# Kernel optimization log

Hardware: AMD Instinct MI355X
Metric: run time of the kernel (lower is better)

The kernel has to match this reference:

```python
import jax, jax.numpy as jnp
import numpy as np

D = 1024   # hidden_dim
F = 4096   # ffn_dim
E = 8      # expert_num
K = 2      # top_k
B, S = 2, 2048

def setup_inputs() -> dict:
    key = jax.random.key(0)
    ks = jax.random.split(key, 5)
    scale = 0.02
    x = jax.random.normal(ks[0], (B, S, D), dtype=jnp.float32)
    gate_w = jax.random.normal(ks[1], (D, E), dtype=jnp.float32) * scale
    w1 = jax.random.normal(ks[2], (E, D, F), dtype=jnp.float32) * scale
    w3 = jax.random.normal(ks[3], (E, D, F), dtype=jnp.float32) * scale
    w2 = jax.random.normal(ks[4], (E, F, D), dtype=jnp.float32) * scale
    return {"x": x, "gate_w": gate_w, "w1": w1, "w3": w3, "w2": w2}

def reference(x, gate_w, w1, w3, w2):
    # x: [B, S, D] -> tokens [T, D]
    Bb, Ss, Dd = x.shape
    xt = x.reshape(-1, Dd)                                  # [T, D]
    T = xt.shape[0]
    # Router: softmax over experts in float32 (matches torch dtype=torch.float)
    router_probs = jax.nn.softmax((xt @ gate_w).astype(jnp.float32), axis=-1)  # [T, E]
    topk_w, topk_idx = jax.lax.top_k(router_probs, K)        # [T, K]
    topk_w = topk_w / topk_w.sum(axis=-1, keepdims=True)
    topk_w = topk_w.astype(x.dtype)
    # Combine weights scattered to dense [T, E] (equivalent to per-expert gather/scatter loop)
    combine = jnp.zeros((T, E), dtype=x.dtype).at[jnp.arange(T)[:, None], topk_idx].add(topk_w)
    # SwishFFN per expert: w2(silu(x w1) * (x w3)), no bias
    h = jax.nn.silu(jnp.einsum('td,edf->etf', xt, w1)) * jnp.einsum('td,edf->etf', xt, w3)  # [E, T, F]
    out_e = jnp.einsum('etf,efd->etd', h, w2)                # [E, T, D]
    out = jnp.einsum('etd,te->td', out_e, combine)           # [T, D]
    return out.reshape(Bb, Ss, Dd), router_probs
```

## Files before the change

### kernel.cpp

```cpp
#include <hip/hip_runtime.h>

typedef unsigned short u16;
typedef unsigned int u32;
typedef __attribute__((ext_vector_type(8))) short bf16x8;
typedef __attribute__((ext_vector_type(4))) float f32x4;
typedef __attribute__((ext_vector_type(4))) int i32x4;
typedef __attribute__((ext_vector_type(2))) unsigned int u32x2;


__device__ __forceinline__ u16 f2bf(float f) {
  u32 u = __builtin_bit_cast(u32, f);
  u += 0x7fffu + ((u >> 16) & 1u);
  return (u16)(u >> 16);
}
__device__ __forceinline__ u32 pack2(u16 a, u16 b) { return (u32)a | ((u32)b << 16); }

__device__ __forceinline__ char* lds_swz(void* base, int row, int byteInRow) {
  return (char*)base + (((row << 7) + byteInRow) ^ ((row & 7) << 4));
}

#define GLL16(g, l) __builtin_amdgcn_global_load_lds( \
    (const __attribute__((address_space(1))) void*)(g), \
    (__attribute__((address_space(3))) void*)(l), 16, 0, 0)

__global__ __launch_bounds__(256) void router_k(
    const float* __restrict__ x, const float* __restrict__ gw,
    float* __restrict__ probs, u16* __restrict__ xb,
    float* __restrict__ wa, int* __restrict__ alist, int* __restrict__ cnt)
{
  const int t = blockIdx.x;
  const int tid = threadIdx.x;
  f32x4 xv = ((const f32x4*)(x + (size_t)t * 1024))[tid];
  u32x2 hb;
  hb[0] = pack2(f2bf(xv[0]), f2bf(xv[1]));
  hb[1] = pack2(f2bf(xv[2]), f2bf(xv[3]));
  *(u32x2*)(xb + (size_t)t * 1024 + tid * 4) = hb;

  float acc[8];
#pragma unroll
  for (int e = 0; e < 8; ++e) acc[e] = 0.f;
  const float* g = gw + tid * 32;
#pragma unroll
  for (int j = 0; j < 4; ++j)
#pragma unroll
    for (int e = 0; e < 8; ++e) acc[e] = fmaf(xv[j], g[j * 8 + e], acc[e]);

#pragma unroll
  for (int e = 0; e < 8; ++e)
    for (int off = 32; off > 0; off >>= 1) acc[e] += __shfl_down(acc[e], off);

  __shared__ float red[4][8];
  const int lane = tid & 63, wid = tid >> 6;
  if (lane == 0) {
#pragma unroll
    for (int e = 0; e < 8; ++e) red[wid][e] = acc[e];
  }
  __syncthreads();
  if (tid == 0) {
    float p[8]; float mx = -1e30f;
#pragma unroll
    for (int e = 0; e < 8; ++e) { p[e] = red[0][e] + red[1][e] + red[2][e] + red[3][e]; mx = fmaxf(mx, p[e]); }
    float s = 0.f;
#pragma unroll
    for (int e = 0; e < 8; ++e) { p[e] = __expf(p[e] - mx); s += p[e]; }
    float inv = 1.f / s;
#pragma unroll
    for (int e = 0; e < 8; ++e) { p[e] *= inv; probs[(size_t)t * 8 + e] = p[e]; }
    int i0 = 0;
#pragma unroll
    for (int e = 1; e < 8; ++e) if (p[e] > p[i0]) i0 = e;
    int i1 = (i0 == 0) ? 1 : 0;
#pragma unroll
    for (int e = 0; e < 8; ++e) if (e != i0 && p[e] > p[i1]) i1 = e;
    float s2 = p[i0] + p[i1];
    int pos0 = atomicAdd(&cnt[i0], 1); alist[i0 * 4096 + pos0] = t * 2;
    int pos1 = atomicAdd(&cnt[i1], 1); alist[i1 * 4096 + pos1] = t * 2 + 1;
    wa[t * 2]     = p[i0] / s2;
    wa[t * 2 + 1] = p[i1] / s2;
  }
}

__global__ __launch_bounds__(256) void wtrans_k(const float* __restrict__ src, u16* __restrict__ dst,
                                               int R, int C)
{
  const int e = blockIdx.z;
  src += (size_t)e * R * C;
  dst += (size_t)e * R * C;
  const int c0 = blockIdx.x * 64, r0 = blockIdx.y * 64;
  __shared__ u16 t[64][72];
  const int tid = threadIdx.x;
  const int rr = (tid >> 4) * 4, cc = (tid & 15) * 4;
  f32x4 v[4];
#pragma unroll
  for (int j = 0; j < 4; ++j) v[j] = *(const f32x4*)(src + (size_t)(r0 + rr + j) * C + c0 + cc);
#pragma unroll
  for (int c = 0; c < 4; ++c) {
    u32x2 p;
    p[0] = pack2(f2bf(v[0][c]), f2bf(v[1][c]));
    p[1] = pack2(f2bf(v[2][c]), f2bf(v[3][c]));
    *(u32x2*)&t[cc + c][rr] = p;
  }
  __syncthreads();
  const int c = tid >> 2, rs = (tid & 3) * 16;
  i32x4 a0 = *(const i32x4*)&t[c][rs];
  i32x4 a1 = *(const i32x4*)&t[c][rs + 8];
  u16* dp = dst + (size_t)(c0 + c) * R + r0 + rs;
  *(i32x4*)dp = a0;
  *(i32x4*)(dp + 8) = a1;
}

__global__ __launch_bounds__(256, 2) void gemm1_k(
    const u16* __restrict__ xb, const u16* __restrict__ w1t, const u16* __restrict__ w3t,
    const int* __restrict__ alist, const int* __restrict__ cnt, u16* __restrict__ H)
{
  const int e = blockIdx.z;
  const int mc = cnt[e];
  const int m0 = blockIdx.y * 128;
  if (m0 >= mc) return;
  const int n0 = blockIdx.x * 64;
  const int tid = threadIdx.x;

  __shared__ u16 As[128 * 64];
  __shared__ u16 Bs[2][64 * 64];
  __shared__ int rowid[128];

  if (tid < 128) rowid[tid] = (m0 + tid < mc) ? alist[e * 4096 + m0 + tid] : -1;
  __syncthreads();

  const int l = tid & 63, w = tid >> 6;
  const u16* wt = (w >> 1) ? w3t : w1t;
  u16* bbase = &Bs[w >> 1][0];

  const u16* aps[4]; const u16* bps[4];
  u16* ald[4]; u16* bld[4];
#pragma unroll
  for (int q = 0; q < 4; ++q) {
    int ra = 32 * w + 8 * q + (l >> 3);
    int id = rowid[ra];
    aps[q] = xb + (size_t)(id < 0 ? 0 : (id >> 1)) * 1024 + ((l & 7) ^ (ra & 7)) * 8;
    ald[q] = As + (32 * w + 8 * q) * 64;
    int rb = 32 * (w & 1) + 8 * q + (l >> 3);
    bps[q] = wt + (size_t)e * 4194304 + (size_t)(n0 + rb) * 1024 + ((l & 7) ^ (rb & 7)) * 8;
    bld[q] = bbase + (32 * (w & 1) + 8 * q) * 64;
  }

  const int wm = (w >> 1) * 64, wn = (w & 1) * 32;
  const int l15 = l & 15, lg = l >> 4;

  f32x4 acc1[4][2], acc3[4][2];
  const f32x4 zf = {0.f, 0.f, 0.f, 0.f};
#pragma unroll
  for (int mi = 0; mi < 4; ++mi) { acc1[mi][0] = zf; acc1[mi][1] = zf; acc3[mi][0] = zf; acc3[mi][1] = zf; }

  for (int kt = 0; kt < 16; ++kt) {
    const int ko = kt * 64;
#pragma unroll
    for (int q = 0; q < 4; ++q) GLL16(aps[q] + ko, ald[q]);
#pragma unroll
    for (int q = 0; q < 4; ++q) GLL16(bps[q] + ko, bld[q]);
    __syncthreads();
#pragma unroll
    for (int ks = 0; ks < 2; ++ks) {
      const int kb = ks * 64 + lg * 16;
      bf16x8 af[4];
#pragma unroll
      for (int mi = 0; mi < 4; ++mi)
        af[mi] = *(const bf16x8*)lds_swz(As, wm + mi * 16 + l15, kb);
#pragma unroll
      for (int ni = 0; ni < 2; ++ni) {
        bf16x8 b1 = *(const bf16x8*)lds_swz(&Bs[0][0], wn + ni * 16 + l15, kb);
        bf16x8 b3 = *(const bf16x8*)lds_swz(&Bs[1][0], wn + ni * 16 + l15, kb);
#pragma unroll
        for (int mi = 0; mi < 4; ++mi) {
          acc1[mi][ni] = __builtin_amdgcn_mfma_f32_16x16x32_bf16(af[mi], b1, acc1[mi][ni], 0, 0, 0);
          acc3[mi][ni] = __builtin_amdgcn_mfma_f32_16x16x32_bf16(af[mi], b3, acc3[mi][ni], 0, 0, 0);
        }
      }
    }
    __syncthreads();
  }

#pragma unroll
  for (int mi = 0; mi < 4; ++mi) {
    const int rb = wm + mi * 16 + lg * 4;
#pragma unroll
    for (int ni = 0; ni < 2; ++ni) {
      const int col = n0 + wn + ni * 16 + l15;
      f32x4 c1 = acc1[mi][ni], c3 = acc3[mi][ni];
#pragma unroll
      for (int j = 0; j < 4; ++j) {
        int id = rowid[rb + j];
        if (id >= 0) {
          float a = c1[j];
          float h = (a / (1.f + __expf(-a))) * c3[j];
          H[(size_t)id * 4096 + col] = f2bf(h);
        }
      }
    }
  }
}

__global__ __launch_bounds__(256, 2) void gemm2_k(
    const u16* __restrict__ H, const u16* __restrict__ w2t,
    const int* __restrict__ alist, const int* __restrict__ cnt,
    const float* __restrict__ wa, float* __restrict__ out)
{
  const int e = blockIdx.z;
  const int mc = cnt[e];
  const int yy = blockIdx.y;
  const int kh = yy & 1;
  const int m0 = (yy >> 1) * 128;
  if (m0 >= mc) return;
  const int n0 = blockIdx.x * 128;
  const int tid = threadIdx.x;

  __shared__ u16 As[128 * 64];
  __shared__ u16 Bs[128 * 64];
  __shared__ int rowid[128];
  __shared__ float rw[128];

  if (tid < 128) {
    int id = (m0 + tid < mc) ? alist[e * 4096 + m0 + tid] : -1;
    rowid[tid] = id;
    rw[tid] = (id >= 0) ? wa[id] : 0.f;
  }
  __syncthreads();

  const int l = tid & 63, w = tid >> 6;
  const size_t kbase = (size_t)kh * 2048;
  const u16* aps[4]; const u16* bps[4];
  u16* ald[4]; u16* bld[4];
#pragma unroll
  for (int q = 0; q < 4; ++q) {
    int ra = 32 * w + 8 * q + (l >> 3);
    int id = rowid[ra];
    aps[q] = H + (size_t)(id < 0 ? 0 : id) * 4096 + kbase + ((l & 7) ^ (ra & 7)) * 8;
    ald[q] = As + (32 * w + 8 * q) * 64;
    int rb = 32 * w + 8 * q + (l >> 3);
    bps[q] = w2t + (size_t)e * 4194304 + (size_t)(n0 + rb) * 4096 + kbase + ((l & 7) ^ (rb & 7)) * 8;
    bld[q] = Bs + (32 * w + 8 * q) * 64;
  }

  const int wm = (w >> 1) * 64, wn = (w & 1) * 64;
  const int l15 = l & 15, lg = l >> 4;

  f32x4 acc[4][4];
  const f32x4 zf = {0.f, 0.f, 0.f, 0.f};
#pragma unroll
  for (int mi = 0; mi < 4; ++mi)
#pragma unroll
    for (int ni = 0; ni < 4; ++ni) acc[mi][ni] = zf;

  for (int kt = 0; kt < 32; ++kt) {
    const int ko = kt * 64;
#pragma unroll
    for (int q = 0; q < 4; ++q) GLL16(aps[q] + ko, ald[q]);
#pragma unroll
    for (int q = 0; q < 4; ++q) GLL16(bps[q] + ko, bld[q]);
    __syncthreads();
#pragma unroll
    for (int ks = 0; ks < 2; ++ks) {
      const int kb = ks * 64 + lg * 16;
      bf16x8 af[4];
#pragma unroll
      for (int mi = 0; mi < 4; ++mi)
        af[mi] = *(const bf16x8*)lds_swz(As, wm + mi * 16 + l15, kb);
#pragma unroll
      for (int ni = 0; ni < 4; ++ni) {
        bf16x8 bfb = *(const bf16x8*)lds_swz(Bs, wn + ni * 16 + l15, kb);
#pragma unroll
        for (int mi = 0; mi < 4; ++mi)
          acc[mi][ni] = __builtin_amdgcn_mfma_f32_16x16x32_bf16(af[mi], bfb, acc[mi][ni], 0, 0, 0);
      }
    }
    __syncthreads();
  }

#pragma unroll
  for (int mi = 0; mi < 4; ++mi) {
    const int rb = wm + mi * 16 + lg * 4;
#pragma unroll
    for (int ni = 0; ni < 4; ++ni) {
      const int col = n0 + wn + ni * 16 + l15;
      f32x4 c = acc[mi][ni];
#pragma unroll
      for (int j = 0; j < 4; ++j) {
        int rr = rb + j;
        int id = rowid[rr];
        if (id >= 0)
          unsafeAtomicAdd(&out[(size_t)(id >> 1) * 1024 + col], c[j] * rw[rr]);
      }
    }
  }
}

extern "C" void kernel_launch(void* const* d_in, const int* in_sizes, int n_in,
                              void* d_out, int out_size, void* d_ws, size_t ws_size,
                              hipStream_t stream)
{
  (void)in_sizes; (void)n_in; (void)out_size; (void)ws_size;
  const float* x  = (const float*)d_in[0];
  const float* gw = (const float*)d_in[1];
  const float* w1 = (const float*)d_in[2];
  const float* w3 = (const float*)d_in[3];
  const float* w2 = (const float*)d_in[4];
  float* out   = (float*)d_out;
  float* probs = out + (size_t)4096 * 1024;

  const size_t MB = (size_t)1 << 20;
  char* ws = (char*)d_ws;
  u16*   xb    = (u16*)(ws);
  u16*   H     = (u16*)(ws + 8 * MB);
  u16*   w1t   = (u16*)(ws + 72 * MB);
  u16*   w3t   = (u16*)(ws + 136 * MB);
  u16*   w2t   = (u16*)(ws + 200 * MB);
  float* wa    = (float*)(ws + 264 * MB);
  int*   alist = (int*)(ws + 264 * MB + 32768);
  int*   cnt   = (int*)(ws + 264 * MB + 32768 + 131072);

  hipMemsetAsync(cnt, 0, 8 * sizeof(int), stream);
  hipMemsetAsync(out, 0, (size_t)4096 * 1024 * sizeof(float), stream);
  wtrans_k<<<dim3(64, 16, 8), 256, 0, stream>>>(w1, w1t, 1024, 4096);
  wtrans_k<<<dim3(64, 16, 8), 256, 0, stream>>>(w3, w3t, 1024, 4096);
  wtrans_k<<<dim3(16, 64, 8), 256, 0, stream>>>(w2, w2t, 4096, 1024);
  router_k<<<4096, 256, 0, stream>>>(x, gw, probs, xb, wa, alist, cnt);
  gemm1_k<<<dim3(64, 32, 8), 256, 0, stream>>>(xb, w1t, w3t, alist, cnt, H);
  gemm2_k<<<dim3(8, 64, 8), 256, 0, stream>>>(H, w2t, alist, cnt, wa, out);
}
```

Baseline: 501.3 us.

## Double-buffer weight tiles and register-prefetch gathered A rows in both expert GEMMs

Both expert GEMM kernels move from a single-buffered load-sync-compute loop to a software pipeline. B tiles are double-buffered in LDS through async global-to-LDS loads. A rows are prefetched into registers and written to LDS after compute, so memory latency overlaps the MFMA work. The three weight-transpose launches are merged into one kernel and the occupancy hint goes from 2 to 3 blocks. The cost is more LDS per block, hand-written waitcnt counts that must match the compiler's load ordering, and register pressure that may cause spills at the higher occupancy target.

```diff
diff --git a/kernel.cpp b/kernel.cpp
--- a/kernel.cpp
+++ b/kernel.cpp
@@ -80,13 +80,31 @@
   }
 }
 
-__global__ __launch_bounds__(256) void wtrans_k(const float* __restrict__ src, u16* __restrict__ dst,
-                                               int R, int C)
-{
-  const int e = blockIdx.z;
-  src += (size_t)e * R * C;
-  dst += (size_t)e * R * C;
-  const int c0 = blockIdx.x * 64, r0 = blockIdx.y * 64;
+__global__ __launch_bounds__(256) void wprep_k(
+    const float* __restrict__ w1, const float* __restrict__ w3, const float* __restrict__ w2,
+    u16* __restrict__ w1t, u16* __restrict__ w3t, u16* __restrict__ w2t)
+{
+  const int bid = blockIdx.x;
+  const float* src; u16* dst; int R, C, x, y, e;
+  if (bid < 16384) {
+    int sel = bid >> 13;
+    int t0 = bid & 8191;
+    e = t0 >> 10;
+    int rem = t0 & 1023;
+    x = rem & 63; y = rem >> 6;
+    R = 1024; C = 4096;
+    src = (sel ? w3 : w1); dst = (sel ? w3t : w1t);
+  } else {
+    int t0 = bid - 16384;
+    e = t0 >> 10;
+    int rem = t0 & 1023;
+    x = rem & 15; y = rem >> 4;
+    R = 4096; C = 1024;
+    src = w2; dst = w2t;
+  }
+  src += (size_t)e * 4194304;
+  dst += (size_t)e * 4194304;
+  const int c0 = x * 64, r0 = y * 64;
   __shared__ u16 t[64][72];
   const int tid = threadIdx.x;
   const int rr = (tid >> 4) * 4, cc = (tid & 15) * 4;
@@ -109,7 +127,7 @@
   *(i32x4*)(dp + 8) = a1;
 }
 
-__global__ __launch_bounds__(256, 2) void gemm1_k(
+__global__ __launch_bounds__(256, 3) void gemm1_k(
     const u16* __restrict__ xb, const u16* __restrict__ w1t, const u16* __restrict__ w3t,
     const int* __restrict__ alist, const int* __restrict__ cnt, u16* __restrict__ H)
 {
@@ -121,27 +139,28 @@
   const int tid = threadIdx.x;
 
   __shared__ u16 As[128 * 64];
-  __shared__ u16 Bs[2][64 * 64];
+  __shared__ u16 Bs[2][2][64 * 64];
   __shared__ int rowid[128];
 
   if (tid < 128) rowid[tid] = (m0 + tid < mc) ? alist[e * 4096 + m0 + tid] : -1;
   __syncthreads();
 
   const int l = tid & 63, w = tid >> 6;
+
+  const int arow = tid >> 1, ah = tid & 1;
+  const int id_a = rowid[arow];
+  const u16* asrc = xb + (size_t)(id_a < 0 ? 0 : (id_a >> 1)) * 1024 + ah * 32;
+  char* awr[4];
+#pragma unroll
+  for (int j = 0; j < 4; ++j) awr[j] = lds_swz(As, arow, ah * 64 + j * 16);
+
   const u16* wt = (w >> 1) ? w3t : w1t;
-  u16* bbase = &Bs[w >> 1][0];
-
-  const u16* aps[4]; const u16* bps[4];
-  u16* ald[4]; u16* bld[4];
+  const u16* bps[4]; u16* bl0[4];
 #pragma unroll
   for (int q = 0; q < 4; ++q) {
-    int ra = 32 * w + 8 * q + (l >> 3);
-    int id = rowid[ra];
-    aps[q] = xb + (size_t)(id < 0 ? 0 : (id >> 1)) * 1024 + ((l & 7) ^ (ra & 7)) * 8;
-    ald[q] = As + (32 * w + 8 * q) * 64;
     int rb = 32 * (w & 1) + 8 * q + (l >> 3);
     bps[q] = wt + (size_t)e * 4194304 + (size_t)(n0 + rb) * 1024 + ((l & 7) ^ (rb & 7)) * 8;
-    bld[q] = bbase + (32 * (w & 1) + 8 * q) * 64;
+    bl0[q] = &Bs[0][w >> 1][(32 * (w & 1) + 8 * q) * 64];
   }
 
   const int wm = (w >> 1) * 64, wn = (w & 1) * 32;
@@ -152,33 +171,53 @@
 #pragma unroll
   for (int mi = 0; mi < 4; ++mi) { acc1[mi][0] = zf; acc1[mi][1] = zf; acc3[mi][0] = zf; acc3[mi][1] = zf; }
 
-  for (int kt = 0; kt < 16; ++kt) {
-    const int ko = kt * 64;
-#pragma unroll
-    for (int q = 0; q < 4; ++q) GLL16(aps[q] + ko, ald[q]);
-#pragma unroll
-    for (int q = 0; q < 4; ++q) GLL16(bps[q] + ko, bld[q]);
-    __syncthreads();
-#pragma unroll
-    for (int ks = 0; ks < 2; ++ks) {
-      const int kb = ks * 64 + lg * 16;
-      bf16x8 af[4];
-#pragma unroll
-      for (int mi = 0; mi < 4; ++mi)
-        af[mi] = *(const bf16x8*)lds_swz(As, wm + mi * 16 + l15, kb);
-#pragma unroll
-      for (int ni = 0; ni < 2; ++ni) {
-        bf16x8 b1 = *(const bf16x8*)lds_swz(&Bs[0][0], wn + ni * 16 + l15, kb);
-        bf16x8 b3 = *(const bf16x8*)lds_swz(&Bs[1][0], wn + ni * 16 + l15, kb);
-#pragma unroll
-        for (int mi = 0; mi < 4; ++mi) {
-          acc1[mi][ni] = __builtin_amdgcn_mfma_f32_16x16x32_bf16(af[mi], b1, acc1[mi][ni], 0, 0, 0);
-          acc3[mi][ni] = __builtin_amdgcn_mfma_f32_16x16x32_bf16(af[mi], b3, acc3[mi][ni], 0, 0, 0);
-        }
-      }
-    }
-    __syncthreads();
-  }
+  i32x4 a2[4];
+#pragma unroll
+  for (int j = 0; j < 4; ++j) a2[j] = *(const i32x4*)(asrc + j * 8);
+#pragma unroll
+  for (int q = 0; q < 4; ++q) GLL16(bps[q], bl0[q]);
+  asm volatile("s_waitcnt vmcnt(4)" ::: "memory");
+#pragma unroll
+  for (int j = 0; j < 4; ++j) *(i32x4*)awr[j] = a2[j];
+
+#define G1_COMPUTE(BO)                                                          \
+  _Pragma("unroll")                                                             \
+  for (int ks = 0; ks < 2; ++ks) {                                              \
+    const int kb = ks * 64 + lg * 16;                                           \
+    bf16x8 af[4];                                                               \
+    _Pragma("unroll")                                                           \
+    for (int mi = 0; mi < 4; ++mi)                                              \
+      af[mi] = *(const bf16x8*)lds_swz(As, wm + mi * 16 + l15, kb);             \
+    _Pragma("unroll")                                                           \
+    for (int ni = 0; ni < 2; ++ni) {                                            \
+      bf16x8 b1 = *(const bf16x8*)lds_swz(&Bs[0][0][0] + (BO), wn + ni * 16 + l15, kb);        \
+      bf16x8 b3 = *(const bf16x8*)lds_swz(&Bs[0][0][0] + (BO) + 4096, wn + ni * 16 + l15, kb); \
+      _Pragma("unroll")                                                         \
+      for (int mi = 0; mi < 4; ++mi) {                                          \
+        acc1[mi][ni] = __builtin_amdgcn_mfma_f32_16x16x32_bf16(af[mi], b1, acc1[mi][ni], 0, 0, 0); \
+        acc3[mi][ni] = __builtin_amdgcn_mfma_f32_16x16x32_bf16(af[mi], b3, acc3[mi][ni], 0, 0, 0); \
+      }                                                                         \
+    }                                                                           \
+  }
+
+#pragma unroll 2
+  for (int kt = 0; kt < 15; ++kt) {
+    const int ko = (kt + 1) * 64;
+#pragma unroll
+    for (int j = 0; j < 4; ++j) a2[j] = *(const i32x4*)(asrc + ko + j * 8);
+#pragma unroll
+    for (int q = 0; q < 4; ++q) GLL16(bps[q] + ko, bl0[q] + ((kt + 1) & 1) * 8192);
+    asm volatile("s_waitcnt vmcnt(8) lgkmcnt(0)" ::: "memory");
+    __builtin_amdgcn_s_barrier();
+    G1_COMPUTE((kt & 1) * 8192);
+    __builtin_amdgcn_s_barrier();
+    asm volatile("s_waitcnt vmcnt(4)" ::: "memory");
+#pragma unroll
+    for (int j = 0; j < 4; ++j) *(i32x4*)awr[j] = a2[j];
+  }
+  asm volatile("s_waitcnt vmcnt(0) lgkmcnt(0)" ::: "memory");
+  __builtin_amdgcn_s_barrier();
+  G1_COMPUTE(8192);
 
 #pragma unroll
   for (int mi = 0; mi < 4; ++mi) {
@@ -200,7 +239,7 @@
   }
 }
 
-__global__ __launch_bounds__(256, 2) void gemm2_k(
+__global__ __launch_bounds__(256, 3) void gemm2_k(
     const u16* __restrict__ H, const u16* __restrict__ w2t,
     const int* __restrict__ alist, const int* __restrict__ cnt,
     const float* __restrict__ wa, float* __restrict__ out)
@@ -215,7 +254,7 @@
   const int tid = threadIdx.x;
 
   __shared__ u16 As[128 * 64];
-  __shared__ u16 Bs[128 * 64];
+  __shared__ u16 Bs[2][128 * 64];
   __shared__ int rowid[128];
   __shared__ float rw[128];
 
@@ -228,17 +267,20 @@
 
   const int l = tid & 63, w = tid >> 6;
   const size_t kbase = (size_t)kh * 2048;
-  const u16* aps[4]; const u16* bps[4];
-  u16* ald[4]; u16* bld[4];
+
+  const int arow = tid >> 1, ah = tid & 1;
+  const int id_a = rowid[arow];
+  const u16* asrc = H + (size_t)(id_a < 0 ? 0 : id_a) * 4096 + kbase + ah * 32;
+  char* awr[4];
+#pragma unroll
+  for (int j = 0; j < 4; ++j) awr[j] = lds_swz(As, arow, ah * 64 + j * 16);
+
+  const u16* bps[4]; u16* bl0[4];
 #pragma unroll
   for (int q = 0; q < 4; ++q) {
-    int ra = 32 * w + 8 * q + (l >> 3);
-    int id = rowid[ra];
-    aps[q] = H + (size_t)(id < 0 ? 0 : id) * 4096 + kbase + ((l & 7) ^ (ra & 7)) * 8;
-    ald[q] = As + (32 * w + 8 * q) * 64;
     int rb = 32 * w + 8 * q + (l >> 3);
     bps[q] = w2t + (size_t)e * 4194304 + (size_t)(n0 + rb) * 4096 + kbase + ((l & 7) ^ (rb & 7)) * 8;
-    bld[q] = Bs + (32 * w + 8 * q) * 64;
+    bl0[q] = &Bs[0][(32 * w + 8 * q) * 64];
   }
 
   const int wm = (w >> 1) * 64, wn = (w & 1) * 64;
@@ -251,30 +293,50 @@
 #pragma unroll
     for (int ni = 0; ni < 4; ++ni) acc[mi][ni] = zf;
 
-  for (int kt = 0; kt < 32; ++kt) {
-    const int ko = kt * 64;
-#pragma unroll
-    for (int q = 0; q < 4; ++q) GLL16(aps[q] + ko, ald[q]);
-#pragma unroll
-    for (int q = 0; q < 4; ++q) GLL16(bps[q] + ko, bld[q]);
-    __syncthreads();
-#pragma unroll
-    for (int ks = 0; ks < 2; ++ks) {
-      const int kb = ks * 64 + lg * 16;
-      bf16x8 af[4];
-#pragma unroll
-      for (int mi = 0; mi < 4; ++mi)
-        af[mi] = *(const bf16x8*)lds_swz(As, wm + mi * 16 + l15, kb);
-#pragma unroll
-      for (int ni = 0; ni < 4; ++ni) {
-        bf16x8 bfb = *(const bf16x8*)lds_swz(Bs, wn + ni * 16 + l15, kb);
-#pragma unroll
-        for (int mi = 0; mi < 4; ++mi)
-          acc[mi][ni] = __builtin_amdgcn_mfma_f32_16x16x32_bf16(af[mi], bfb, acc[mi][ni], 0, 0, 0);
-      }
-    }
-    __syncthreads();
-  }
+  i32x4 a2[4];
+#pragma unroll
+  for (int j = 0; j < 4; ++j) a2[j] = *(const i32x4*)(asrc + j * 8);
+#pragma unroll
+  for (int q = 0; q < 4; ++q) GLL16(bps[q], bl0[q]);
+  asm volatile("s_waitcnt vmcnt(4)" ::: "memory");
+#pragma unroll
+  for (int j = 0; j < 4; ++j) *(i32x4*)awr[j] = a2[j];
+
+#define G2_COMPUTE(BO)                                                          \
+  _Pragma("unroll")                                                             \
+  for (int ks = 0; ks < 2; ++ks) {                                              \
+    const int kb = ks * 64 + lg * 16;                                           \
+    bf16x8 af[4];                                                               \
+    _Pragma("unroll")                                                           \
+    for (int mi = 0; mi < 4; ++mi)                                              \
+      af[mi] = *(const bf16x8*)lds_swz(As, wm + mi * 16 + l15, kb);             \
+    _Pragma("unroll")                                                           \
+    for (int ni = 0; ni < 4; ++ni) {                                            \
+      bf16x8 bfb = *(const bf16x8*)lds_swz(&Bs[0][0] + (BO), wn + ni * 16 + l15, kb); \
+      _Pragma("unroll")                                                         \
+      for (int mi = 0; mi < 4; ++mi)                                            \
+        acc[mi][ni] = __builtin_amdgcn_mfma_f32_16x16x32_bf16(af[mi], bfb, acc[mi][ni], 0, 0, 0); \
+    }                                                                           \
+  }
+
+#pragma unroll 2
+  for (int kt = 0; kt < 31; ++kt) {
+    const int ko = (kt + 1) * 64;
+#pragma unroll
+    for (int j = 0; j < 4; ++j) a2[j] = *(const i32x4*)(asrc + ko + j * 8);
+#pragma unroll
+    for (int q = 0; q < 4; ++q) GLL16(bps[q] + ko, bl0[q] + ((kt + 1) & 1) * 8192);
+    asm volatile("s_waitcnt vmcnt(8) lgkmcnt(0)" ::: "memory");
+    __builtin_amdgcn_s_barrier();
+    G2_COMPUTE((kt & 1) * 8192);
+    __builtin_amdgcn_s_barrier();
+    asm volatile("s_waitcnt vmcnt(4)" ::: "memory");
+#pragma unroll
+    for (int j = 0; j < 4; ++j) *(i32x4*)awr[j] = a2[j];
+  }
+  asm volatile("s_waitcnt vmcnt(0) lgkmcnt(0)" ::: "memory");
+  __builtin_amdgcn_s_barrier();
+  G2_COMPUTE(8192);
 
 #pragma unroll
   for (int mi = 0; mi < 4; ++mi) {
@@ -320,10 +382,8 @@
 
   hipMemsetAsync(cnt, 0, 8 * sizeof(int), stream);
   hipMemsetAsync(out, 0, (size_t)4096 * 1024 * sizeof(float), stream);
-  wtrans_k<<<dim3(64, 16, 8), 256, 0, stream>>>(w1, w1t, 1024, 4096);
-  wtrans_k<<<dim3(64, 16, 8), 256, 0, stream>>>(w3, w3t, 1024, 4096);
-  wtrans_k<<<dim3(16, 64, 8), 256, 0, stream>>>(w2, w2t, 4096, 1024);
   router_k<<<4096, 256, 0, stream>>>(x, gw, probs, xb, wa, alist, cnt);
+  wprep_k<<<24576, 256, 0, stream>>>(w1, w3, w2, w1t, w3t, w2t);
   gemm1_k<<<dim3(64, 32, 8), 256, 0, stream>>>(xb, w1t, w3t, alist, cnt, H);
   gemm2_k<<<dim3(8, 64, 8), 256, 0, stream>>>(H, w2t, alist, cnt, wa, out);
 }
```

Result: slower. 525.2 us (+4.8%).

## Merge w1/w3 transpose with router and overlap w2 transpose with gemm1

Applied to the files above, without the earlier changes.

The separate w1/w3 transpose kernels and the router are folded into one launch that picks its role from the block index. The w2 transpose runs inside gemm1 on extra blocks (bx>=64), so it overlaps the first expert GEMM instead of running as its own kernel. This cuts launch count and fills idle CUs during gemm1, since many gemm1 blocks exit early for sparse experts. The cost is a larger grid and shared-memory layout for gemm1, and the extra transpose blocks compete with GEMM blocks for bandwidth.

```diff
diff --git a/kernel.cpp b/kernel.cpp
--- a/kernel.cpp
+++ b/kernel.cpp
@@ -23,71 +23,10 @@
     (const __attribute__((address_space(1))) void*)(g), \
     (__attribute__((address_space(3))) void*)(l), 16, 0, 0)
 
-__global__ __launch_bounds__(256) void router_k(
-    const float* __restrict__ x, const float* __restrict__ gw,
-    float* __restrict__ probs, u16* __restrict__ xb,
-    float* __restrict__ wa, int* __restrict__ alist, int* __restrict__ cnt)
-{
-  const int t = blockIdx.x;
-  const int tid = threadIdx.x;
-  f32x4 xv = ((const f32x4*)(x + (size_t)t * 1024))[tid];
-  u32x2 hb;
-  hb[0] = pack2(f2bf(xv[0]), f2bf(xv[1]));
-  hb[1] = pack2(f2bf(xv[2]), f2bf(xv[3]));
-  *(u32x2*)(xb + (size_t)t * 1024 + tid * 4) = hb;
-
-  float acc[8];
-#pragma unroll
-  for (int e = 0; e < 8; ++e) acc[e] = 0.f;
-  const float* g = gw + tid * 32;
-#pragma unroll
-  for (int j = 0; j < 4; ++j)
-#pragma unroll
-    for (int e = 0; e < 8; ++e) acc[e] = fmaf(xv[j], g[j * 8 + e], acc[e]);
-
-#pragma unroll
-  for (int e = 0; e < 8; ++e)
-    for (int off = 32; off > 0; off >>= 1) acc[e] += __shfl_down(acc[e], off);
-
-  __shared__ float red[4][8];
-  const int lane = tid & 63, wid = tid >> 6;
-  if (lane == 0) {
-#pragma unroll
-    for (int e = 0; e < 8; ++e) red[wid][e] = acc[e];
-  }
-  __syncthreads();
-  if (tid == 0) {
-    float p[8]; float mx = -1e30f;
-#pragma unroll
-    for (int e = 0; e < 8; ++e) { p[e] = red[0][e] + red[1][e] + red[2][e] + red[3][e]; mx = fmaxf(mx, p[e]); }
-    float s = 0.f;
-#pragma unroll
-    for (int e = 0; e < 8; ++e) { p[e] = __expf(p[e] - mx); s += p[e]; }
-    float inv = 1.f / s;
-#pragma unroll
-    for (int e = 0; e < 8; ++e) { p[e] *= inv; probs[(size_t)t * 8 + e] = p[e]; }
-    int i0 = 0;
-#pragma unroll
-    for (int e = 1; e < 8; ++e) if (p[e] > p[i0]) i0 = e;
-    int i1 = (i0 == 0) ? 1 : 0;
-#pragma unroll
-    for (int e = 0; e < 8; ++e) if (e != i0 && p[e] > p[i1]) i1 = e;
-    float s2 = p[i0] + p[i1];
-    int pos0 = atomicAdd(&cnt[i0], 1); alist[i0 * 4096 + pos0] = t * 2;
-    int pos1 = atomicAdd(&cnt[i1], 1); alist[i1 * 4096 + pos1] = t * 2 + 1;
-    wa[t * 2]     = p[i0] / s2;
-    wa[t * 2 + 1] = p[i1] / s2;
-  }
-}
-
-__global__ __launch_bounds__(256) void wtrans_k(const float* __restrict__ src, u16* __restrict__ dst,
-                                               int R, int C)
-{
-  const int e = blockIdx.z;
-  src += (size_t)e * R * C;
-  dst += (size_t)e * R * C;
-  const int c0 = blockIdx.x * 64, r0 = blockIdx.y * 64;
-  __shared__ u16 t[64][72];
+__device__ __forceinline__ void wtrans_tile(const float* __restrict__ src, u16* __restrict__ dst,
+                                            int R, int C, int c0, int r0, void* lds)
+{
+  u16 (*t)[72] = (u16 (*)[72])lds;
   const int tid = threadIdx.x;
   const int rr = (tid >> 4) * 4, cc = (tid & 15) * 4;
   f32x4 v[4];
@@ -109,27 +48,117 @@
   *(i32x4*)(dp + 8) = a1;
 }
 
-__global__ __launch_bounds__(256, 2) void gemm1_k(
+__global__ __launch_bounds__(256) void prep13_router_k(
+    const float* __restrict__ w1, const float* __restrict__ w3,
+    u16* __restrict__ w1t, u16* __restrict__ w3t,
+    const float* __restrict__ x, const float* __restrict__ gw,
+    float* __restrict__ probs, u16* __restrict__ xb,
+    float* __restrict__ wa, int* __restrict__ alist, int* __restrict__ cnt)
+{
+  __shared__ __align__(16) char smem[9216];
+  const int bid = blockIdx.x;
+  if (bid < 16384) {
+    const int sel = bid >> 13;
+    const int t0 = bid & 8191;
+    const int e = t0 >> 10;
+    const int rem = t0 & 1023;
+    const int xt = rem & 63, yt = rem >> 6;
+    const float* src = (sel ? w3 : w1) + (size_t)e * 4194304;
+    u16* dst = (sel ? w3t : w1t) + (size_t)e * 4194304;
+    wtrans_tile(src, dst, 1024, 4096, xt * 64, yt * 64, smem);
+    return;
+  }
+  const int t = bid - 16384;
+  const int tid = threadIdx.x;
+  f32x4 xv = ((const f32x4*)(x + (size_t)t * 1024))[tid];
+  u32x2 hb;
+  hb[0] = pack2(f2bf(xv[0]), f2bf(xv[1]));
+  hb[1] = pack2(f2bf(xv[2]), f2bf(xv[3]));
+  *(u32x2*)(xb + (size_t)t * 1024 + tid * 4) = hb;
+
+  float acc[8];
+#pragma unroll
+  for (int e = 0; e < 8; ++e) acc[e] = 0.f;
+  const float* g = gw + tid * 32;
+#pragma unroll
+  for (int j = 0; j < 4; ++j)
+#pragma unroll
+    for (int e = 0; e < 8; ++e) acc[e] = fmaf(xv[j], g[j * 8 + e], acc[e]);
+
+#pragma unroll
+  for (int e = 0; e < 8; ++e)
+    for (int off = 32; off > 0; off >>= 1) acc[e] += __shfl_down(acc[e], off);
+
+  float* red = (float*)smem;
+  const int lane = tid & 63, wid = tid >> 6;
+  if (lane == 0) {
+#pragma unroll
+    for (int e = 0; e < 8; ++e) red[wid * 8 + e] = acc[e];
+  }
+  __syncthreads();
+  if (tid == 0) {
+    float p[8]; float mx = -1e30f;
+#pragma unroll
+    for (int e = 0; e < 8; ++e) { p[e] = red[e] + red[8 + e] + red[16 + e] + red[24 + e]; mx = fmaxf(mx, p[e]); }
+    float s = 0.f;
+#pragma unroll
+    for (int e = 0; e < 8; ++e) { p[e] = __expf(p[e] - mx); s += p[e]; }
+    float inv = 1.f / s;
+#pragma unroll
+    for (int e = 0; e < 8; ++e) { p[e] *= inv; probs[(size_t)t * 8 + e] = p[e]; }
+    int i0 = 0;
+#pragma unroll
+    for (int e = 1; e < 8; ++e) if (p[e] > p[i0]) i0 = e;
+    int i1 = (i0 == 0) ? 1 : 0;
+#pragma unroll
+    for (int e = 0; e < 8; ++e) if (e != i0 && p[e] > p[i1]) i1 = e;
+    float s2 = p[i0] + p[i1];
+    int pos0 = atomicAdd(&cnt[i0], 1); alist[i0 * 4096 + pos0] = t * 2;
+    int pos1 = atomicAdd(&cnt[i1], 1); alist[i1 * 4096 + pos1] = t * 2 + 1;
+    wa[t * 2]     = p[i0] / s2;
+    wa[t * 2 + 1] = p[i1] / s2;
+  }
+}
+
+__global__ __launch_bounds__(256, 2) void gemm1w2_k(
     const u16* __restrict__ xb, const u16* __restrict__ w1t, const u16* __restrict__ w3t,
-    const int* __restrict__ alist, const int* __restrict__ cnt, u16* __restrict__ H)
-{
+    const int* __restrict__ alist, const int* __restrict__ cnt, u16* __restrict__ H,
+    const float* __restrict__ w2, u16* __restrict__ w2t)
+{
+  __shared__ __align__(16) char smem[33280];
   const int e = blockIdx.z;
+  const int bx = blockIdx.x;
+
+  if (bx >= 64) {
+    const float* src = w2 + (size_t)e * 4194304;
+    u16* dst = w2t + (size_t)e * 4194304;
+    const int slot = (bx - 64) * 32 + blockIdx.y;
+#pragma unroll
+    for (int j = 0; j < 4; ++j) {
+      const int tj = slot * 4 + j;
+      const int cx = tj & 15, ry = tj >> 4;
+      wtrans_tile(src, dst, 4096, 1024, cx * 64, ry * 64, smem);
+      __syncthreads();
+    }
+    return;
+  }
+
+  u16* As = (u16*)smem;
+  u16* Bs = (u16*)(smem + 16384);
+  int* rowid = (int*)(smem + 32768);
+
   const int mc = cnt[e];
   const int m0 = blockIdx.y * 128;
   if (m0 >= mc) return;
-  const int n0 = blockIdx.x * 64;
+  const int n0 = bx * 64;
   const int tid = threadIdx.x;
-
-  __shared__ u16 As[128 * 64];
-  __shared__ u16 Bs[2][64 * 64];
-  __shared__ int rowid[128];
 
   if (tid < 128) rowid[tid] = (m0 + tid < mc) ? alist[e * 4096 + m0 + tid] : -1;
   __syncthreads();
 
   const int l = tid & 63, w = tid >> 6;
   const u16* wt = (w >> 1) ? w3t : w1t;
-  u16* bbase = &Bs[w >> 1][0];
+  u16* bbase = Bs + (w >> 1) * 4096;
 
   const u16* aps[4]; const u16* bps[4];
   u16* ald[4]; u16* bld[4];
@@ -168,8 +197,8 @@
         af[mi] = *(const bf16x8*)lds_swz(As, wm + mi * 16 + l15, kb);
 #pragma unroll
       for (int ni = 0; ni < 2; ++ni) {
-        bf16x8 b1 = *(const bf16x8*)lds_swz(&Bs[0][0], wn + ni * 16 + l15, kb);
-        bf16x8 b3 = *(const bf16x8*)lds_swz(&Bs[1][0], wn + ni * 16 + l15, kb);
+        bf16x8 b1 = *(const bf16x8*)lds_swz(Bs, wn + ni * 16 + l15, kb);
+        bf16x8 b3 = *(const bf16x8*)lds_swz(Bs + 4096, wn + ni * 16 + l15, kb);
 #pragma unroll
         for (int mi = 0; mi < 4; ++mi) {
           acc1[mi][ni] = __builtin_amdgcn_mfma_f32_16x16x32_bf16(af[mi], b1, acc1[mi][ni], 0, 0, 0);
@@ -320,10 +349,7 @@
 
   hipMemsetAsync(cnt, 0, 8 * sizeof(int), stream);
   hipMemsetAsync(out, 0, (size_t)4096 * 1024 * sizeof(float), stream);
-  wtrans_k<<<dim3(64, 16, 8), 256, 0, stream>>>(w1, w1t, 1024, 4096);
-  wtrans_k<<<dim3(64, 16, 8), 256, 0, stream>>>(w3, w3t, 1024, 4096);
-  wtrans_k<<<dim3(16, 64, 8), 256, 0, stream>>>(w2, w2t, 4096, 1024);
-  router_k<<<4096, 256, 0, stream>>>(x, gw, probs, xb, wa, alist, cnt);
-  gemm1_k<<<dim3(64, 32, 8), 256, 0, stream>>>(xb, w1t, w3t, alist, cnt, H);
+  prep13_router_k<<<20480, 256, 0, stream>>>(w1, w3, w1t, w3t, x, gw, probs, xb, wa, alist, cnt);
+  gemm1w2_k<<<dim3(72, 32, 8), 256, 0, stream>>>(xb, w1t, w3t, alist, cnt, H, w2, w2t);
   gemm2_k<<<dim3(8, 64, 8), 256, 0, stream>>>(H, w2t, alist, cnt, wa, out);
 }
```

Result: faster. 485.5 us (-3.2%).
